# Kernel tuning notes

Hardware: AMD Instinct MI355X
Metric: run time of the kernel (lower is better)

The kernel has to match this reference:

```python
import jax, jax.numpy as jnp
import numpy as np

B, C, H, W = 16, 8, 512, 512
EPS_TH = 1e-14

def setup_inputs() -> dict:
    key = jax.random.key(0)
    x = jax.random.normal(key, (B, C, H, W), dtype=jnp.float32)
    alpha = jnp.full((1,), 0.95, dtype=jnp.float32)
    beta = jnp.full((1,), 8.0, dtype=jnp.float32)
    return {"x": x, "alpha": alpha, "beta": beta}

def reference(x, alpha, beta):
    b, c, h, w = x.shape
    x2 = x.reshape(b * c, h * w)
    # torch.nanquantile with default linear interpolation == jnp.nanquantile
    i1 = jnp.nanquantile(x2, 0.01, axis=1, keepdims=True)   # [B*C, 1]
    i99 = jnp.nanquantile(x2, 0.99, axis=1, keepdims=True)  # [B*C, 1]
    th = (i1 + (i99 - i1) * alpha).reshape(b, c, 1, 1)      # broadcast instead of tile
    mask = (th > EPS_TH).astype(x.dtype)
    th_new = th * mask + (1.0 - mask)
    gate = 1.0 / (1.0 + jnp.exp(-(beta / th_new * (jnp.abs(x) - th * mask))))
    return jax.nn.relu(x) * gate
```

## Files before the change

kernel.cpp:

```cpp
#include <hip/hip_runtime.h>


#define ROWS 128
#define NPR  262144
#define BINS 8192
#define SHIFT 19
#define CAP  4096
#define CBUF 2048

#define K_LO 2621u
#define K_HI 259521u

#define OFF_GH   0
#define OFF_GCNT (ROWS*2*BINS)
#define OFF_SB   (OFF_GCNT + 256)
#define OFF_CAND (OFF_SB + ROWS*8)
#define OFF_QV   (OFF_CAND + ROWS*2*CAP)

__device__ __forceinline__ unsigned keyOf(float f) {
    unsigned u = __float_as_uint(f);
    return (u & 0x80000000u) ? ~u : (u | 0x80000000u);
}
__device__ __forceinline__ float keyToFloat(unsigned k) {
    unsigned u = (k & 0x80000000u) ? (k & 0x7fffffffu) : ~k;
    return __uint_as_float(u);
}

__global__ __launch_bounds__(1024) void k_hist(const float* __restrict__ x,
                                               unsigned* __restrict__ gh) {
    __shared__ unsigned lh[BINS];
    for (int i = threadIdx.x; i < BINS; i += 1024) lh[i] = 0;
    __syncthreads();
    const int row  = blockIdx.x >> 1;
    const int half = blockIdx.x & 1;
    const float4* xr = (const float4*)(x + (size_t)row * NPR + (size_t)half * (NPR / 2));
    const int NV = NPR / 2 / 4;
    for (int i = threadIdx.x; i < NV; i += 1024) {
        float4 v = xr[i];
        atomicAdd(&lh[keyOf(v.x) >> SHIFT], 1u);
        atomicAdd(&lh[keyOf(v.y) >> SHIFT], 1u);
        atomicAdd(&lh[keyOf(v.z) >> SHIFT], 1u);
        atomicAdd(&lh[keyOf(v.w) >> SHIFT], 1u);
    }
    __syncthreads();
    unsigned* h = gh + (size_t)blockIdx.x * BINS;
    for (int i = threadIdx.x; i < BINS; i += 1024) h[i] = lh[i];
}

__global__ __launch_bounds__(256) void k_scan(const unsigned* __restrict__ gh,
                                              unsigned* __restrict__ sbinfo) {
    const int row = blockIdx.x;
    const int tid = threadIdx.x;
    const unsigned* h0 = gh + (size_t)(row * 2) * BINS;
    const unsigned* h1 = h0 + BINS;
    __shared__ unsigned part[256];
    __shared__ unsigned sb[8];
    const int CH = BINS / 256;
    int base = tid * CH;
    unsigned loc[CH];
    unsigned s = 0;
    #pragma unroll
    for (int i = 0; i < CH; ++i) { loc[i] = h0[base + i] + h1[base + i]; s += loc[i]; }
    part[tid] = s;
    __syncthreads();
    if (tid == 0) {
        unsigned run = 0;
        for (int t = 0; t < 256; ++t) { unsigned tmp = part[t]; part[t] = run; run += tmp; }
    }
    __syncthreads();
    {
        unsigned cum = part[tid];
        const unsigned targets[4] = {K_LO, K_LO + 1u, K_HI, K_HI + 1u};
        for (int i = 0; i < CH; ++i) {
            unsigned c = loc[i];
            if (c) {
                #pragma unroll
                for (int t = 0; t < 4; ++t) {
                    if (targets[t] >= cum && targets[t] < cum + c) {
                        if      (t == 0) { sb[0] = base + i; sb[2] = cum; }
                        else if (t == 1) { sb[1] = base + i; }
                        else if (t == 2) { sb[3] = base + i; sb[5] = cum; }
                        else             { sb[4] = base + i; }
                    }
                }
            }
            cum += c;
        }
    }
    __syncthreads();
    if (tid == 0) {
        unsigned* r = sbinfo + row * 8;
        r[0] = sb[0] << SHIFT;
        r[1] = ((sb[1] + 1u) << SHIFT) - 1u;
        r[2] = sb[2];
        r[3] = sb[3] << SHIFT;
        r[4] = ((sb[4] + 1u) << SHIFT) - 1u;
        r[5] = sb[5];
    }
}

__global__ __launch_bounds__(256) void k_collect(const float* __restrict__ x,
                                                 const unsigned* __restrict__ sbinfo,
                                                 unsigned* __restrict__ gcnt,
                                                 unsigned* __restrict__ candg) {
    __shared__ unsigned buf0[CBUF], buf1[CBUF];
    __shared__ unsigned lc[2];
    __shared__ unsigned gbase[2];
    const int row = blockIdx.x >> 4;
    const int blk = blockIdx.x & 15;
    if (threadIdx.x < 2) lc[threadIdx.x] = 0;
    __syncthreads();
    const unsigned* r = sbinfo + row * 8;
    const unsigned klo0 = r[0], khi0 = r[1], klo1 = r[3], khi1 = r[4];
    const float4* xr = (const float4*)(x + (size_t)row * NPR + (size_t)blk * (NPR / 16));
    const int NV = NPR / 16 / 4;
    for (int i = threadIdx.x; i < NV; i += 256) {
        float4 v = xr[i];
        float vv[4] = {v.x, v.y, v.z, v.w};
        #pragma unroll
        for (int j = 0; j < 4; ++j) {
            unsigned key = keyOf(vv[j]);
            if (key >= klo0 && key <= khi0) {
                unsigned p = atomicAdd(&lc[0], 1u);
                if (p < CBUF) buf0[p] = key;
            }
            if (key >= klo1 && key <= khi1) {
                unsigned p = atomicAdd(&lc[1], 1u);
                if (p < CBUF) buf1[p] = key;
            }
        }
    }
    __syncthreads();
    if (threadIdx.x < 2) {
        unsigned n = lc[threadIdx.x]; if (n > CBUF) n = CBUF;
        gbase[threadIdx.x] = atomicAdd(&gcnt[row * 2 + threadIdx.x], n);
    }
    __syncthreads();
    unsigned n0 = lc[0] > CBUF ? CBUF : lc[0];
    unsigned n1 = lc[1] > CBUF ? CBUF : lc[1];
    unsigned* c0 = candg + (size_t)(row * 2) * CAP;
    unsigned* c1 = c0 + CAP;
    for (unsigned i = threadIdx.x; i < n0; i += 256) {
        unsigned p = gbase[0] + i; if (p < CAP) c0[p] = buf0[i];
    }
    for (unsigned i = threadIdx.x; i < n1; i += 256) {
        unsigned p = gbase[1] + i; if (p < CAP) c1[p] = buf1[i];
    }
}

__global__ __launch_bounds__(256) void k_select(const unsigned* __restrict__ candg,
                                                const unsigned* __restrict__ gcnt,
                                                const unsigned* __restrict__ sbinfo,
                                                float* __restrict__ qv) {
    const int rq  = blockIdx.x;
    const int row = rq >> 1;
    const int iq  = rq & 1;
    const int tid = threadIdx.x;
    __shared__ unsigned keys[CAP];
    __shared__ unsigned sh[256];
    __shared__ unsigned svar[4];
    unsigned m = gcnt[rq]; if (m > CAP) m = CAP;
    const unsigned* cand = candg + (size_t)rq * CAP;
    for (unsigned i = tid; i < m; i += 256) keys[i] = cand[i];
    __syncthreads();

    const unsigned cb   = sbinfo[row * 8 + (iq ? 5 : 2)];
    const unsigned t_lo = (iq ? K_HI : K_LO) - cb;
    unsigned prefix = 0, trem = t_lo, cntEq = 0;
    for (int p = 3; p >= 0; --p) {
        sh[tid] = 0;
        __syncthreads();
        for (unsigned i = tid; i < m; i += 256) {
            unsigned key = keys[i];
            bool match = (p == 3) || ((key >> ((p + 1) * 8)) == (prefix >> ((p + 1) * 8)));
            if (match) atomicAdd(&sh[(key >> (p * 8)) & 255u], 1u);
        }
        __syncthreads();
        if (tid == 0) {
            unsigned cum = 0;
            for (int b = 0; b < 256; ++b) {
                unsigned c = sh[b];
                if (trem >= cum && trem < cum + c) { svar[0] = (unsigned)b; svar[1] = cum; svar[2] = c; break; }
                cum += c;
            }
        }
        __syncthreads();
        prefix |= svar[0] << (p * 8);
        trem   -= svar[1];
        cntEq   = svar[2];
        __syncthreads();
    }
    unsigned vlo_key = prefix;
    unsigned cntLess = t_lo - trem;
    unsigned vhi_key;
    if (t_lo + 1u < cntLess + cntEq) {
        vhi_key = vlo_key;
    } else {
        if (tid == 0) svar[3] = 0xFFFFFFFFu;
        __syncthreads();
        for (unsigned i = tid; i < m; i += 256) {
            unsigned key = keys[i];
            if (key > vlo_key) atomicMin(&svar[3], key);
        }
        __syncthreads();
        vhi_key = svar[3];
    }
    if (tid == 0) {
        double frac = iq ? (0.99 * (double)(NPR - 1) - (double)K_HI)
                         : (0.01 * (double)(NPR - 1) - (double)K_LO);
        double vlo = (double)keyToFloat(vlo_key);
        double vhi = (double)keyToFloat(vhi_key);
        qv[rq] = (float)(vlo + (vhi - vlo) * frac);
    }
}

__global__ __launch_bounds__(256) void k_out(const float* __restrict__ x,
                                             const float* __restrict__ alpha,
                                             const float* __restrict__ beta,
                                             const float* __restrict__ qv,
                                             float* __restrict__ out) {
    const int row = blockIdx.x >> 4;
    float q0 = qv[row * 2], q1 = qv[row * 2 + 1];
    float a = alpha[0], bt = beta[0];
    float th = q0 + (q1 - q0) * a;
    bool  msk = th > 1e-14f;
    float thn = msk ? th : 1.0f;
    float thm = msk ? th : 0.0f;
    float nsc = -(bt / thn) * 1.4426950408889634f;
    const float4* xv = (const float4*)x + (size_t)blockIdx.x * 4096;
    float4*       ov = (float4*)out     + (size_t)blockIdx.x * 4096;
    #pragma unroll 4
    for (int k = 0; k < 16; ++k) {
        int i = k * 256 + threadIdx.x;
        float4 v = xv[i];
        float4 o;
        o.x = v.x > 0.f ? v.x * __builtin_amdgcn_rcpf(1.f + __builtin_amdgcn_exp2f(nsc * (fabsf(v.x) - thm))) : 0.f;
        o.y = v.y > 0.f ? v.y * __builtin_amdgcn_rcpf(1.f + __builtin_amdgcn_exp2f(nsc * (fabsf(v.y) - thm))) : 0.f;
        o.z = v.z > 0.f ? v.z * __builtin_amdgcn_rcpf(1.f + __builtin_amdgcn_exp2f(nsc * (fabsf(v.z) - thm))) : 0.f;
        o.w = v.w > 0.f ? v.w * __builtin_amdgcn_rcpf(1.f + __builtin_amdgcn_exp2f(nsc * (fabsf(v.w) - thm))) : 0.f;
        ov[i] = o;
    }
}

extern "C" void kernel_launch(void* const* d_in, const int* in_sizes, int n_in,
                              void* d_out, int out_size, void* d_ws, size_t ws_size,
                              hipStream_t stream) {
    const float* x     = (const float*)d_in[0];
    const float* alpha = (const float*)d_in[1];
    const float* beta  = (const float*)d_in[2];
    float* out = (float*)d_out;
    unsigned* ws = (unsigned*)d_ws;
    unsigned* gh     = ws + OFF_GH;
    unsigned* gcnt   = ws + OFF_GCNT;
    unsigned* sbinfo = ws + OFF_SB;
    unsigned* candg  = ws + OFF_CAND;
    float*    qv     = (float*)(ws + OFF_QV);
    hipMemsetAsync(gcnt, 0, 256 * sizeof(unsigned), stream);
    k_hist   <<<ROWS * 2,  1024, 0, stream>>>(x, gh);
    k_scan   <<<ROWS,      256,  0, stream>>>(gh, sbinfo);
    k_collect<<<ROWS * 16, 256,  0, stream>>>(x, sbinfo, gcnt, candg);
    k_select <<<ROWS * 2,  256,  0, stream>>>(candg, gcnt, sbinfo, qv);
    k_out    <<<ROWS * 16, 256,  0, stream>>>(x, alpha, beta, qv, out);
}
```

Before: 357.2 us.

## Privatize histogram per half-block, fold memset into scan, nontemporal output stores

The histogram kernel now keeps two shared-memory sub-histograms, one per 512-thread half, to reduce LDS atomic contention, and sums them when writing out. The separate memset of the candidate counters is dropped and the zeroing moves into k_scan, saving one stream operation. The output kernel uses nontemporal stores with a higher unroll so the write stream bypasses cache. In exchange, the histogram doubles its LDS footprint to 64 KB, which may limit occupancy.

```diff
diff --git a/kernel.cpp b/kernel.cpp
--- a/kernel.cpp
+++ b/kernel.cpp
@@ -17,6 +17,8 @@
 #define OFF_CAND (OFF_SB + ROWS*8)
 #define OFF_QV   (OFF_CAND + ROWS*2*CAP)
 
+typedef float  f32x4 __attribute__((ext_vector_type(4)));
+
 __device__ __forceinline__ unsigned keyOf(float f) {
     unsigned u = __float_as_uint(f);
     return (u & 0x80000000u) ? ~u : (u | 0x80000000u);
@@ -28,29 +30,33 @@
 
 __global__ __launch_bounds__(1024) void k_hist(const float* __restrict__ x,
                                                unsigned* __restrict__ gh) {
-    __shared__ unsigned lh[BINS];
-    for (int i = threadIdx.x; i < BINS; i += 1024) lh[i] = 0;
-    __syncthreads();
+    __shared__ unsigned lh[2][BINS];
+    unsigned* flat = &lh[0][0];
+    for (int i = threadIdx.x; i < 2 * BINS; i += 1024) flat[i] = 0;
+    __syncthreads();
+    unsigned* myh = lh[threadIdx.x >> 9];
     const int row  = blockIdx.x >> 1;
     const int half = blockIdx.x & 1;
     const float4* xr = (const float4*)(x + (size_t)row * NPR + (size_t)half * (NPR / 2));
     const int NV = NPR / 2 / 4;
     for (int i = threadIdx.x; i < NV; i += 1024) {
         float4 v = xr[i];
-        atomicAdd(&lh[keyOf(v.x) >> SHIFT], 1u);
-        atomicAdd(&lh[keyOf(v.y) >> SHIFT], 1u);
-        atomicAdd(&lh[keyOf(v.z) >> SHIFT], 1u);
-        atomicAdd(&lh[keyOf(v.w) >> SHIFT], 1u);
+        atomicAdd(&myh[keyOf(v.x) >> SHIFT], 1u);
+        atomicAdd(&myh[keyOf(v.y) >> SHIFT], 1u);
+        atomicAdd(&myh[keyOf(v.z) >> SHIFT], 1u);
+        atomicAdd(&myh[keyOf(v.w) >> SHIFT], 1u);
     }
     __syncthreads();
     unsigned* h = gh + (size_t)blockIdx.x * BINS;
-    for (int i = threadIdx.x; i < BINS; i += 1024) h[i] = lh[i];
+    for (int i = threadIdx.x; i < BINS; i += 1024) h[i] = lh[0][i] + lh[1][i];
 }
 
 __global__ __launch_bounds__(256) void k_scan(const unsigned* __restrict__ gh,
-                                              unsigned* __restrict__ sbinfo) {
+                                              unsigned* __restrict__ sbinfo,
+                                              unsigned* __restrict__ gcnt) {
     const int row = blockIdx.x;
     const int tid = threadIdx.x;
+    if (tid < 2) gcnt[row * 2 + tid] = 0;
     const unsigned* h0 = gh + (size_t)(row * 2) * BINS;
     const unsigned* h1 = h0 + BINS;
     __shared__ unsigned part[256];
@@ -71,6 +77,7 @@
     {
         unsigned cum = part[tid];
         const unsigned targets[4] = {K_LO, K_LO + 1u, K_HI, K_HI + 1u};
+        #pragma unroll
         for (int i = 0; i < CH; ++i) {
             unsigned c = loc[i];
             if (c) {
@@ -228,17 +235,17 @@
     float thm = msk ? th : 0.0f;
     float nsc = -(bt / thn) * 1.4426950408889634f;
     const float4* xv = (const float4*)x + (size_t)blockIdx.x * 4096;
-    float4*       ov = (float4*)out     + (size_t)blockIdx.x * 4096;
-    #pragma unroll 4
+    f32x4*        ov = (f32x4*)out      + (size_t)blockIdx.x * 4096;
+    #pragma unroll 8
     for (int k = 0; k < 16; ++k) {
         int i = k * 256 + threadIdx.x;
         float4 v = xv[i];
-        float4 o;
+        f32x4 o;
         o.x = v.x > 0.f ? v.x * __builtin_amdgcn_rcpf(1.f + __builtin_amdgcn_exp2f(nsc * (fabsf(v.x) - thm))) : 0.f;
         o.y = v.y > 0.f ? v.y * __builtin_amdgcn_rcpf(1.f + __builtin_amdgcn_exp2f(nsc * (fabsf(v.y) - thm))) : 0.f;
         o.z = v.z > 0.f ? v.z * __builtin_amdgcn_rcpf(1.f + __builtin_amdgcn_exp2f(nsc * (fabsf(v.z) - thm))) : 0.f;
         o.w = v.w > 0.f ? v.w * __builtin_amdgcn_rcpf(1.f + __builtin_amdgcn_exp2f(nsc * (fabsf(v.w) - thm))) : 0.f;
-        ov[i] = o;
+        __builtin_nontemporal_store(o, &ov[i]);
     }
 }
 
@@ -255,9 +262,8 @@
     unsigned* sbinfo = ws + OFF_SB;
     unsigned* candg  = ws + OFF_CAND;
     float*    qv     = (float*)(ws + OFF_QV);
-    hipMemsetAsync(gcnt, 0, 256 * sizeof(unsigned), stream);
     k_hist   <<<ROWS * 2,  1024, 0, stream>>>(x, gh);
-    k_scan   <<<ROWS,      256,  0, stream>>>(gh, sbinfo);
+    k_scan   <<<ROWS,      256,  0, stream>>>(gh, sbinfo, gcnt);
     k_collect<<<ROWS * 16, 256,  0, stream>>>(x, sbinfo, gcnt, candg);
     k_select <<<ROWS * 2,  256,  0, stream>>>(candg, gcnt, sbinfo, qv);
     k_out    <<<ROWS * 16, 256,  0, stream>>>(x, alpha, beta, qv, out);
```

New measurement: 354.7 us. Within noise of the previous version (-0.7%).
